# Performance work log

Hardware: AMD Instinct MI355X
Metric: run time of the kernel (lower is better)

## Reference

```python
import jax, jax.numpy as jnp
import numpy as np

UNITS = 512
DIM = 64
BATCH = 2048


def setup_inputs() -> dict:
    key = jax.random.key(0)
    kx, k1, k2 = jax.random.split(key, 3)
    # glorot_uniform limit for (units, dim)
    limit = float(np.sqrt(6.0 / (UNITS + DIM)))
    x = jax.random.normal(kx, (BATCH, DIM), dtype=jnp.float32)
    q1 = jax.random.uniform(k1, (UNITS, DIM), dtype=jnp.float32, minval=-limit, maxval=limit)
    q2 = jax.random.uniform(k2, (UNITS, DIM), dtype=jnp.float32, minval=-limit, maxval=limit)
    r = jnp.ones((UNITS,), dtype=jnp.float32)
    return {"x": x, "q1": q1, "q2": q2, "r": r}


def reference(x, q1, q2, r):
    n = x.shape[-1]
    q12 = q2 - q1                                   # (U, n)
    q12_norm = jnp.linalg.norm(q12, axis=1)         # (U,)
    # scalar projection coefficient: (x - q1) . q12  -> (B, U)
    s = jnp.einsum('bn,un->bu', x, q12) - jnp.sum(q1 * q12, axis=1)
    # projection vector k = (s / ||q12||) * q12  -> (B, U, n)
    kv = (s / q12_norm)[..., None] * q12[None, :, :]
    temp1 = jnp.sum(kv * q12, axis=-1)              # (B, U)
    k_norm = jnp.linalg.norm(kv, axis=-1)           # (B, U)
    temp2 = k_norm / q12_norm                       # (B, U)
    # branchless select replacing the scatter/gather mask logic:
    #   temp1 < 0            -> l = 1
    #   temp1>=0 & temp2<1   -> l = k_norm
    #   else                 -> l = 0
    l = jnp.where(temp1 < 0, 1.0, jnp.where(temp2 < 1, k_norm, 0.0))  # (B, U)
    center = l[..., None] * q1 + (1.0 - l)[..., None] * q2            # (B, U, n)
    d = x[:, None, :] - center                                        # (B, U, n)
    y = -jnp.sum(d * d, axis=-1) / (n * jnp.square(r))                # (B, U)
    return jnp.exp(y)  # activation='exponential'
```

## Files before the change

kernel.cpp:

```cpp
#include <hip/hip_runtime.h>

#define BATCH 2048
#define UNITS 512
#define DIM   64
#define TB    64
#define TU    32
#define XS    68
#define QS    36

extern "C" __global__ void __launch_bounds__(256, 2)
sausage_v3(const float* __restrict__ x, const float* __restrict__ q1,
           const float* __restrict__ q2, const float* __restrict__ r,
           float* __restrict__ out)
{
  __shared__ float sx [64 * XS];
  __shared__ float sq1[64 * QS];
  __shared__ float sq2[64 * QS];
  __shared__ float Lt[TU], Lqn[TU], Lw[TU], Lnn[TU], Lq2n[TU], Linv[TU];
  __shared__ float Lxn[TB];

  const int tid  = threadIdx.x;
  const int lane = tid & 63;
  const int wid  = tid >> 6;
  const int b0   = blockIdx.x * TB;
  const int u0   = blockIdx.y * TU;

  float rv = 1.0f;
  if (tid < TU) rv = r[u0 + tid];

  {
    const int rg = tid >> 4;
    const int ks = tid & 15;
    const float4 v0 = *(const float4*)(x + (size_t)(b0 + 4*rg + 0) * DIM + 4*ks);
    const float4 v1 = *(const float4*)(x + (size_t)(b0 + 4*rg + 1) * DIM + 4*ks);
    const float4 v2 = *(const float4*)(x + (size_t)(b0 + 4*rg + 2) * DIM + 4*ks);
    const float4 v3 = *(const float4*)(x + (size_t)(b0 + 4*rg + 3) * DIM + 4*ks);
    *(float4*)(sx + (4*ks+0)*XS + 4*rg) = make_float4(v0.x, v1.x, v2.x, v3.x);
    *(float4*)(sx + (4*ks+1)*XS + 4*rg) = make_float4(v0.y, v1.y, v2.y, v3.y);
    *(float4*)(sx + (4*ks+2)*XS + 4*rg) = make_float4(v0.z, v1.z, v2.z, v3.z);
    *(float4*)(sx + (4*ks+3)*XS + 4*rg) = make_float4(v0.w, v1.w, v2.w, v3.w);

    const float* qsrc = (tid & 128) ? q2 : q1;
    float*       qdst = (tid & 128) ? sq2 : sq1;
    const int ug8 = (tid >> 4) & 7;
    const float4 w0 = *(const float4*)(qsrc + (size_t)(u0 + 4*ug8 + 0) * DIM + 4*ks);
    const float4 w1 = *(const float4*)(qsrc + (size_t)(u0 + 4*ug8 + 1) * DIM + 4*ks);
    const float4 w2 = *(const float4*)(qsrc + (size_t)(u0 + 4*ug8 + 2) * DIM + 4*ks);
    const float4 w3 = *(const float4*)(qsrc + (size_t)(u0 + 4*ug8 + 3) * DIM + 4*ks);
    *(float4*)(qdst + (4*ks+0)*QS + 4*ug8) = make_float4(w0.x, w1.x, w2.x, w3.x);
    *(float4*)(qdst + (4*ks+1)*QS + 4*ug8) = make_float4(w0.y, w1.y, w2.y, w3.y);
    *(float4*)(qdst + (4*ks+2)*QS + 4*ug8) = make_float4(w0.z, w1.z, w2.z, w3.z);
    *(float4*)(qdst + (4*ks+3)*QS + 4*ug8) = make_float4(w0.w, w1.w, w2.w, w3.w);
  }
  __syncthreads();

  if (wid == 0) {
    const int u = lane & 31;
    const int h = lane >> 5;
    float w = 0.0f, nn = 0.0f, q2n = 0.0f;
    #pragma unroll
    for (int m = 0; m < 32; ++m) {
      const int k = 32*h + m;
      const float a = sq1[k*QS + u];
      const float c = sq2[k*QS + u];
      const float d = c - a;
      w   = fmaf(c, d, w);
      nn  = fmaf(d, d, nn);
      q2n = fmaf(c, c, q2n);
    }
    w   += __shfl_xor(w, 32);
    nn  += __shfl_xor(nn, 32);
    q2n += __shfl_xor(q2n, 32);
    if (h == 0) {
      Lt[u]   = w - nn;
      Lqn[u]  = sqrtf(nn);
      Lw[u]   = w;
      Lnn[u]  = nn;
      Lq2n[u] = q2n;
      Linv[u] = 1.0f / (64.0f * rv * rv);
    }
  } else if (wid == 1) {
    const int b = lane;
    float s0 = 0.f, s1 = 0.f, s2 = 0.f, s3 = 0.f;
    #pragma unroll
    for (int k = 0; k < 64; k += 4) {
      const float a0 = sx[(k+0)*XS + b];
      const float a1 = sx[(k+1)*XS + b];
      const float a2 = sx[(k+2)*XS + b];
      const float a3 = sx[(k+3)*XS + b];
      s0 = fmaf(a0, a0, s0); s1 = fmaf(a1, a1, s1);
      s2 = fmaf(a2, a2, s2); s3 = fmaf(a3, a3, s3);
    }
    Lxn[b] = (s0 + s1) + (s2 + s3);
  }
  __syncthreads();

  const int ug = tid & 15;
  const int bg = tid >> 4;
  const float* px = sx  + 4*bg;
  const float* p1 = sq1 + 2*ug;
  const float* p2 = sq2 + 2*ug;

  float d1[4][2] = {{0.f,0.f},{0.f,0.f},{0.f,0.f},{0.f,0.f}};
  float d2[4][2] = {{0.f,0.f},{0.f,0.f},{0.f,0.f},{0.f,0.f}};

  #pragma unroll
  for (int k = 0; k < 64; ++k) {
    const float4 xv = *(const float4*)(px + k*XS);
    const float2 av = *(const float2*)(p1 + k*QS);
    const float2 cv = *(const float2*)(p2 + k*QS);
    const float xs0 = xv.x, xs1 = xv.y, xs2 = xv.z, xs3 = xv.w;
    d1[0][0] = fmaf(xs0, av.x, d1[0][0]);  d1[0][1] = fmaf(xs0, av.y, d1[0][1]);
    d1[1][0] = fmaf(xs1, av.x, d1[1][0]);  d1[1][1] = fmaf(xs1, av.y, d1[1][1]);
    d1[2][0] = fmaf(xs2, av.x, d1[2][0]);  d1[2][1] = fmaf(xs2, av.y, d1[2][1]);
    d1[3][0] = fmaf(xs3, av.x, d1[3][0]);  d1[3][1] = fmaf(xs3, av.y, d1[3][1]);
    d2[0][0] = fmaf(xs0, cv.x, d2[0][0]);  d2[0][1] = fmaf(xs0, cv.y, d2[0][1]);
    d2[1][0] = fmaf(xs1, cv.x, d2[1][0]);  d2[1][1] = fmaf(xs1, cv.y, d2[1][1]);
    d2[2][0] = fmaf(xs2, cv.x, d2[2][0]);  d2[2][1] = fmaf(xs2, cv.y, d2[2][1]);
    d2[3][0] = fmaf(xs3, cv.x, d2[3][0]);  d2[3][1] = fmaf(xs3, cv.y, d2[3][1]);
  }

  float tt[2], qn[2], ww[2], nn2[2], qq[2], iv[2];
  #pragma unroll
  for (int jj = 0; jj < 2; ++jj) {
    const int ul = 2*ug + jj;
    tt[jj] = Lt[ul];  qn[jj] = Lqn[ul];  ww[jj] = Lw[ul];
    nn2[jj] = Lnn[ul]; qq[jj] = Lq2n[ul]; iv[jj] = Linv[ul];
  }
  #pragma unroll
  for (int i = 0; i < 4; ++i) {
    const float xnv = Lxn[4*bg + i];
    float2 o;
    #pragma unroll
    for (int jj = 0; jj < 2; ++jj) {
      const float a = d2[i][jj] - d1[i][jj];
      const float s = a - tt[jj];
      const float l = (s < 0.0f) ? 1.0f : ((s < qn[jj]) ? s : 0.0f);
      const float dsq = fmaf(-2.0f, d2[i][jj], xnv) + qq[jj]
                      + 2.0f * l * (a - ww[jj]) + l * l * nn2[jj];
      (jj ? o.y : o.x) = __expf(-dsq * iv[jj]);
    }
    *(float2*)(out + (size_t)(b0 + 4*bg + i) * UNITS + u0 + 2*ug) = o;
  }
}

extern "C" void kernel_launch(void* const* d_in, const int* in_sizes, int n_in,
                              void* d_out, int out_size, void* d_ws, size_t ws_size,
                              hipStream_t stream) {
  const float* x  = (const float*)d_in[0];
  const float* q1 = (const float*)d_in[1];
  const float* q2 = (const float*)d_in[2];
  const float* r  = (const float*)d_in[3];
  float* out = (float*)d_out;
  dim3 grid(BATCH / TB, UNITS / TU);
  sausage_v3<<<grid, 256, 0, stream>>>(x, q1, q2, r, out);
}
```

Baseline: 12.80 us.

## Compute dot products with bf16 MFMA and swizzled shared-memory staging

Replaces the FP32 scalar FMA inner product over x·q1 and x·q2 with bf16 16x16x32 MFMA instructions. Inputs are converted to bf16 and stored row-major in an XOR-swizzled shared layout, and the per-unit and per-row norms are fused into the load phase, dropping one sync pass. This cuts instruction count in the dot-product loop. The risk is bf16 rounding error in the distance expansion and narrower scalar output stores.

```diff
diff --git a/kernel.cpp b/kernel.cpp
--- a/kernel.cpp
+++ b/kernel.cpp
@@ -5,73 +5,72 @@
 #define DIM   64
 #define TB    64
 #define TU    32
-#define XS    68
-#define QS    36
+
+typedef __attribute__((ext_vector_type(8))) short short8v;
+typedef __attribute__((ext_vector_type(4))) float float4v;
+
+__device__ __forceinline__ unsigned short f2bf(float f) {
+  union { float f; unsigned u; } v; v.f = f;
+  return (unsigned short)((v.u + 0x7FFFu + ((v.u >> 16) & 1u)) >> 16);
+}
+
+__device__ __forceinline__ int swz(int row, int k) {
+  return (row * 64 + k) ^ ((row & 7) << 3);
+}
 
 extern "C" __global__ void __launch_bounds__(256, 2)
-sausage_v3(const float* __restrict__ x, const float* __restrict__ q1,
+sausage_v4(const float* __restrict__ x, const float* __restrict__ q1,
            const float* __restrict__ q2, const float* __restrict__ r,
            float* __restrict__ out)
 {
-  __shared__ float sx [64 * XS];
-  __shared__ float sq1[64 * QS];
-  __shared__ float sq2[64 * QS];
+  __shared__ __align__(16) unsigned short sX [TB * 64];
+  __shared__ __align__(16) unsigned short sQ1[TU * 64];
+  __shared__ __align__(16) unsigned short sQ2[TU * 64];
   __shared__ float Lt[TU], Lqn[TU], Lw[TU], Lnn[TU], Lq2n[TU], Linv[TU];
   __shared__ float Lxn[TB];
 
-  const int tid  = threadIdx.x;
-  const int lane = tid & 63;
-  const int wid  = tid >> 6;
-  const int b0   = blockIdx.x * TB;
-  const int u0   = blockIdx.y * TU;
+  const int tid = threadIdx.x;
+  const int b0  = blockIdx.x * TB;
+  const int u0  = blockIdx.y * TU;
 
-  float rv = 1.0f;
-  if (tid < TU) rv = r[u0 + tid];
-
-  {
-    const int rg = tid >> 4;
-    const int ks = tid & 15;
-    const float4 v0 = *(const float4*)(x + (size_t)(b0 + 4*rg + 0) * DIM + 4*ks);
-    const float4 v1 = *(const float4*)(x + (size_t)(b0 + 4*rg + 1) * DIM + 4*ks);
-    const float4 v2 = *(const float4*)(x + (size_t)(b0 + 4*rg + 2) * DIM + 4*ks);
-    const float4 v3 = *(const float4*)(x + (size_t)(b0 + 4*rg + 3) * DIM + 4*ks);
-    *(float4*)(sx + (4*ks+0)*XS + 4*rg) = make_float4(v0.x, v1.x, v2.x, v3.x);
-    *(float4*)(sx + (4*ks+1)*XS + 4*rg) = make_float4(v0.y, v1.y, v2.y, v3.y);
-    *(float4*)(sx + (4*ks+2)*XS + 4*rg) = make_float4(v0.z, v1.z, v2.z, v3.z);
-    *(float4*)(sx + (4*ks+3)*XS + 4*rg) = make_float4(v0.w, v1.w, v2.w, v3.w);
-
-    const float* qsrc = (tid & 128) ? q2 : q1;
-    float*       qdst = (tid & 128) ? sq2 : sq1;
-    const int ug8 = (tid >> 4) & 7;
-    const float4 w0 = *(const float4*)(qsrc + (size_t)(u0 + 4*ug8 + 0) * DIM + 4*ks);
-    const float4 w1 = *(const float4*)(qsrc + (size_t)(u0 + 4*ug8 + 1) * DIM + 4*ks);
-    const float4 w2 = *(const float4*)(qsrc + (size_t)(u0 + 4*ug8 + 2) * DIM + 4*ks);
-    const float4 w3 = *(const float4*)(qsrc + (size_t)(u0 + 4*ug8 + 3) * DIM + 4*ks);
-    *(float4*)(qdst + (4*ks+0)*QS + 4*ug8) = make_float4(w0.x, w1.x, w2.x, w3.x);
-    *(float4*)(qdst + (4*ks+1)*QS + 4*ug8) = make_float4(w0.y, w1.y, w2.y, w3.y);
-    *(float4*)(qdst + (4*ks+2)*QS + 4*ug8) = make_float4(w0.z, w1.z, w2.z, w3.z);
-    *(float4*)(qdst + (4*ks+3)*QS + 4*ug8) = make_float4(w0.w, w1.w, w2.w, w3.w);
-  }
-  __syncthreads();
-
-  if (wid == 0) {
-    const int u = lane & 31;
-    const int h = lane >> 5;
-    float w = 0.0f, nn = 0.0f, q2n = 0.0f;
+  if (tid < 128) {
+    const int u   = tid >> 2;
+    const int seg = tid & 3;
+    const float* q1p = q1 + (size_t)(u0 + u) * DIM + seg * 16;
+    const float* q2p = q2 + (size_t)(u0 + u) * DIM + seg * 16;
+    float av[16], cv[16];
     #pragma unroll
-    for (int m = 0; m < 32; ++m) {
-      const int k = 32*h + m;
-      const float a = sq1[k*QS + u];
-      const float c = sq2[k*QS + u];
-      const float d = c - a;
-      w   = fmaf(c, d, w);
+    for (int j = 0; j < 4; ++j) {
+      const float4 a4 = reinterpret_cast<const float4*>(q1p)[j];
+      const float4 c4 = reinterpret_cast<const float4*>(q2p)[j];
+      av[4*j+0] = a4.x; av[4*j+1] = a4.y; av[4*j+2] = a4.z; av[4*j+3] = a4.w;
+      cv[4*j+0] = c4.x; cv[4*j+1] = c4.y; cv[4*j+2] = c4.z; cv[4*j+3] = c4.w;
+    }
+    float nn = 0.f, w = 0.f, q2n = 0.f;
+    #pragma unroll
+    for (int j = 0; j < 16; ++j) {
+      const float d = cv[j] - av[j];
       nn  = fmaf(d, d, nn);
-      q2n = fmaf(c, c, q2n);
+      w   = fmaf(cv[j], d, w);
+      q2n = fmaf(cv[j], cv[j], q2n);
     }
-    w   += __shfl_xor(w, 32);
-    nn  += __shfl_xor(nn, 32);
-    q2n += __shfl_xor(q2n, 32);
-    if (h == 0) {
+    #pragma unroll
+    for (int h = 0; h < 2; ++h) {
+      union { unsigned short u16[8]; short8v v; } p1, p2;
+      #pragma unroll
+      for (int j = 0; j < 8; ++j) {
+        p1.u16[j] = f2bf(av[8*h+j]);
+        p2.u16[j] = f2bf(cv[8*h+j]);
+      }
+      const int idx = swz(u, seg * 16 + 8 * h);
+      *reinterpret_cast<short8v*>(&sQ1[idx]) = p1.v;
+      *reinterpret_cast<short8v*>(&sQ2[idx]) = p2.v;
+    }
+    nn  += __shfl_xor(nn, 1);  nn  += __shfl_xor(nn, 2);
+    w   += __shfl_xor(w, 1);   w   += __shfl_xor(w, 2);
+    q2n += __shfl_xor(q2n, 1); q2n += __shfl_xor(q2n, 2);
+    if (seg == 0) {
+      const float rv = r[u0 + u];
       Lt[u]   = w - nn;
       Lqn[u]  = sqrtf(nn);
       Lw[u]   = w;
@@ -79,68 +78,90 @@
       Lq2n[u] = q2n;
       Linv[u] = 1.0f / (64.0f * rv * rv);
     }
-  } else if (wid == 1) {
-    const int b = lane;
-    float s0 = 0.f, s1 = 0.f, s2 = 0.f, s3 = 0.f;
+  } else {
+    const int tt   = tid - 128;
+    const int row  = tt >> 1;
+    const int half = tt & 1;
+    const float* xp = x + (size_t)(b0 + row) * DIM + half * 32;
+    float v[32];
     #pragma unroll
-    for (int k = 0; k < 64; k += 4) {
-      const float a0 = sx[(k+0)*XS + b];
-      const float a1 = sx[(k+1)*XS + b];
-      const float a2 = sx[(k+2)*XS + b];
-      const float a3 = sx[(k+3)*XS + b];
-      s0 = fmaf(a0, a0, s0); s1 = fmaf(a1, a1, s1);
-      s2 = fmaf(a2, a2, s2); s3 = fmaf(a3, a3, s3);
+    for (int j = 0; j < 8; ++j) {
+      const float4 v4 = reinterpret_cast<const float4*>(xp)[j];
+      v[4*j+0] = v4.x; v[4*j+1] = v4.y; v[4*j+2] = v4.z; v[4*j+3] = v4.w;
     }
-    Lxn[b] = (s0 + s1) + (s2 + s3);
+    float xn = 0.f;
+    #pragma unroll
+    for (int j = 0; j < 32; ++j) xn = fmaf(v[j], v[j], xn);
+    #pragma unroll
+    for (int h = 0; h < 4; ++h) {
+      union { unsigned short u16[8]; short8v v; } p;
+      #pragma unroll
+      for (int j = 0; j < 8; ++j) p.u16[j] = f2bf(v[8*h+j]);
+      const int idx = swz(row, half * 32 + 8 * h);
+      *reinterpret_cast<short8v*>(&sX[idx]) = p.v;
+    }
+    xn += __shfl_xor(xn, 1);
+    if (half == 0) Lxn[row] = xn;
   }
   __syncthreads();
 
-  const int ug = tid & 15;
-  const int bg = tid >> 4;
-  const float* px = sx  + 4*bg;
-  const float* p1 = sq1 + 2*ug;
-  const float* p2 = sq2 + 2*ug;
+  const int lane = tid & 63;
+  const int wid  = tid >> 6;
+  const int wr   = wid >> 1;
+  const int wc   = wid & 1;
+  const int l15  = lane & 15;
+  const int lk   = lane >> 4;
+  const int kb   = lk * 8;
 
-  float d1[4][2] = {{0.f,0.f},{0.f,0.f},{0.f,0.f},{0.f,0.f}};
-  float d2[4][2] = {{0.f,0.f},{0.f,0.f},{0.f,0.f},{0.f,0.f}};
+  short8v a_frag[2][2], b1_frag[2], b2_frag[2];
+  const int urow = wc * 16 + l15;
+  #pragma unroll
+  for (int ks = 0; ks < 2; ++ks) {
+    const int qi = swz(urow, ks * 32 + kb);
+    b1_frag[ks] = *reinterpret_cast<const short8v*>(&sQ1[qi]);
+    b2_frag[ks] = *reinterpret_cast<const short8v*>(&sQ2[qi]);
+    #pragma unroll
+    for (int mt = 0; mt < 2; ++mt) {
+      const int mrow = wr * 32 + mt * 16 + l15;
+      a_frag[mt][ks] = *reinterpret_cast<const short8v*>(&sX[swz(mrow, ks * 32 + kb)]);
+    }
+  }
+
+  float4v acc1[2], acc2[2];
+  #pragma unroll
+  for (int mt = 0; mt < 2; ++mt) {
+    acc1[mt] = (float4v){0.f, 0.f, 0.f, 0.f};
+    acc2[mt] = (float4v){0.f, 0.f, 0.f, 0.f};
+  }
+  #pragma unroll
+  for (int mt = 0; mt < 2; ++mt)
+    #pragma unroll
+    for (int ks = 0; ks < 2; ++ks) {
+      acc1[mt] = __builtin_amdgcn_mfma_f32_16x16x32_bf16(a_frag[mt][ks], b1_frag[ks], acc1[mt], 0, 0, 0);
+      acc2[mt] = __builtin_amdgcn_mfma_f32_16x16x32_bf16(a_frag[mt][ks], b2_frag[ks], acc2[mt], 0, 0, 0);
+    }
+
+  const float t_   = Lt[urow];
+  const float qn_  = Lqn[urow];
+  const float w_   = Lw[urow];
+  const float nn_  = Lnn[urow];
+  const float q2n_ = Lq2n[urow];
+  const float inv_ = Linv[urow];
 
   #pragma unroll
-  for (int k = 0; k < 64; ++k) {
-    const float4 xv = *(const float4*)(px + k*XS);
-    const float2 av = *(const float2*)(p1 + k*QS);
-    const float2 cv = *(const float2*)(p2 + k*QS);
-    const float xs0 = xv.x, xs1 = xv.y, xs2 = xv.z, xs3 = xv.w;
-    d1[0][0] = fmaf(xs0, av.x, d1[0][0]);  d1[0][1] = fmaf(xs0, av.y, d1[0][1]);
-    d1[1][0] = fmaf(xs1, av.x, d1[1][0]);  d1[1][1] = fmaf(xs1, av.y, d1[1][1]);
-    d1[2][0] = fmaf(xs2, av.x, d1[2][0]);  d1[2][1] = fmaf(xs2, av.y, d1[2][1]);
-    d1[3][0] = fmaf(xs3, av.x, d1[3][0]);  d1[3][1] = fmaf(xs3, av.y, d1[3][1]);
-    d2[0][0] = fmaf(xs0, cv.x, d2[0][0]);  d2[0][1] = fmaf(xs0, cv.y, d2[0][1]);
-    d2[1][0] = fmaf(xs1, cv.x, d2[1][0]);  d2[1][1] = fmaf(xs1, cv.y, d2[1][1]);
-    d2[2][0] = fmaf(xs2, cv.x, d2[2][0]);  d2[2][1] = fmaf(xs2, cv.y, d2[2][1]);
-    d2[3][0] = fmaf(xs3, cv.x, d2[3][0]);  d2[3][1] = fmaf(xs3, cv.y, d2[3][1]);
-  }
-
-  float tt[2], qn[2], ww[2], nn2[2], qq[2], iv[2];
-  #pragma unroll
-  for (int jj = 0; jj < 2; ++jj) {
-    const int ul = 2*ug + jj;
-    tt[jj] = Lt[ul];  qn[jj] = Lqn[ul];  ww[jj] = Lw[ul];
-    nn2[jj] = Lnn[ul]; qq[jj] = Lq2n[ul]; iv[jj] = Linv[ul];
-  }
-  #pragma unroll
-  for (int i = 0; i < 4; ++i) {
-    const float xnv = Lxn[4*bg + i];
-    float2 o;
+  for (int mt = 0; mt < 2; ++mt) {
+    const int rbase = wr * 32 + mt * 16 + lk * 4;
     #pragma unroll
-    for (int jj = 0; jj < 2; ++jj) {
-      const float a = d2[i][jj] - d1[i][jj];
-      const float s = a - tt[jj];
-      const float l = (s < 0.0f) ? 1.0f : ((s < qn[jj]) ? s : 0.0f);
-      const float dsq = fmaf(-2.0f, d2[i][jj], xnv) + qq[jj]
-                      + 2.0f * l * (a - ww[jj]) + l * l * nn2[jj];
-      (jj ? o.y : o.x) = __expf(-dsq * iv[jj]);
+    for (int j = 0; j < 4; ++j) {
+      const float d1 = acc1[mt][j];
+      const float d2 = acc2[mt][j];
+      const float a  = d2 - d1;
+      const float s  = a - t_;
+      const float l  = (s < 0.0f) ? 1.0f : ((s < qn_) ? s : 0.0f);
+      const float dsq = fmaf(-2.0f, d2, Lxn[rbase + j]) + q2n_
+                      + 2.0f * l * (a - w_) + l * l * nn_;
+      out[(size_t)(b0 + rbase + j) * UNITS + u0 + urow] = __expf(-dsq * inv_);
     }
-    *(float2*)(out + (size_t)(b0 + 4*bg + i) * UNITS + u0 + 2*ug) = o;
   }
 }
 
@@ -152,6 +173,7 @@
   const float* q2 = (const float*)d_in[2];
   const float* r  = (const float*)d_in[3];
   float* out = (float*)d_out;
+  (void)d_ws; (void)ws_size;
   dim3 grid(BATCH / TB, UNITS / TU);
-  sausage_v3<<<grid, 256, 0, stream>>>(x, q1, q2, r, out);
+  sausage_v4<<<grid, 256, 0, stream>>>(x, q1, q2, r, out);
 }
```

Result: faster. 11.51 us (-10.1%).
